# Kernel optimization log

Measured on AMD Instinct MI355X. Metric: run time of the kernel, lower is better.

Reference implementation:

```python
import jax, jax.numpy as jnp
import numpy as np

D_IN, D_HIDDEN, DT_RANK, D_MEM, STEP = 256, 64, 16, 128, 16
B_, L_ = 2, 2048
S = 0.02  # weight init scale

def generate_a(d_in, d_hidden):
    i = jnp.arange(d_in, dtype=jnp.float32)[:, None]
    j = jnp.arange(d_hidden, dtype=jnp.float32)[None, :]
    off = jnp.sqrt(2.0 * i + 1.0) * jnp.sqrt(2.0 * j + 1.0)
    return jnp.where(i == j, i + 1.0, jnp.where(i > j, off, 0.0))

def setup_inputs():
    key = jax.random.key(0)
    ks = jax.random.split(key, 10)
    d_out = 3 * D_HIDDEN + 2 * D_IN + 2 * DT_RANK
    return {
        "x": jax.random.normal(ks[0], (B_, L_, D_IN), jnp.float32),
        "W_xproj": jax.random.normal(ks[1], (D_IN, d_out), jnp.float32) * S,
        "W_dt": jax.random.normal(ks[2], (DT_RANK, D_IN), jnp.float32) * S,
        "b_dt": jnp.full((D_IN,), -11.0, jnp.float32),
        "W_dtl": jax.random.normal(ks[3], (DT_RANK, D_IN), jnp.float32) * S,
        "b_dtl": jnp.full((D_IN,), -11.0, jnp.float32),
        "A": generate_a(D_IN, D_HIDDEN),
        "Dp": jnp.ones((D_IN,), jnp.float32),
        "W_Q": jax.random.normal(ks[4], (D_IN, D_MEM), jnp.float32) * S,
        "b_Q": jnp.zeros((D_MEM,), jnp.float32),
        "W_K": jax.random.normal(ks[5], (D_IN, D_MEM), jnp.float32) * S,
        "b_K": jnp.zeros((D_MEM,), jnp.float32),
        "W_V": jax.random.normal(ks[6], (D_IN, D_MEM), jnp.float32) * S,
        "b_V": jnp.zeros((D_MEM,), jnp.float32),
        "W_O": jax.random.normal(ks[7], (D_MEM, D_IN), jnp.float32) * S,
        "b_O": jnp.zeros((D_IN,), jnp.float32),
    }

def _selective_scan(u, delta, A, Bm, Cm, Dp):
    # u, delta: (b,l,d); A: (d,n); Bm, Cm: (b,l,n)
    dA = jnp.exp(jnp.einsum('bld,dn->bldn', delta, A))          # (b,l,d,n)
    dBu = delta[..., None] * Bm[:, :, None, :] * u[..., None]   # (b,l,d,n)
    def comb(e1, e2):
        a1, b1 = e1
        a2, b2 = e2
        return a2 * a1, a2 * b1 + b2
    _, xs = jax.lax.associative_scan(comb, (dA, dBu), axis=1)   # states (b,l,d,n)
    y = jnp.einsum('bldn,bln->bld', xs, Cm)
    if Dp is not None:
        y = y + u * Dp
    return y

def reference(x, W_xproj, W_dt, b_dt, W_dtl, b_dtl, A, Dp, W_Q, b_Q, W_K, b_K, W_V, b_V, W_O, b_O):
    proj = x @ W_xproj  # (b,l,3n+2d+2r)
    splits = np.cumsum([D_HIDDEN, D_HIDDEN, D_HIDDEN, D_IN, D_IN, DT_RANK]).tolist()
    Bm, Bl, Cm, E, Fg, dt, dtl = jnp.split(proj, splits, axis=-1)
    delta = jax.nn.softplus(dt @ W_dt + b_dt)       # delta_softplus=True folded in
    delta_l = jax.nn.softplus(dtl @ W_dtl + b_dtl)
    y = _selective_scan(x, delta, A, Bm, Cm, Dp)
    y_local = _selective_scan(x, delta_l, A, Bl, jnp.ones_like(Bl), None)  # C=ones, D=None
    memory = y_local[:, ::STEP, :]                  # strided checkpoints (b,m,d)
    Q = x @ W_Q + b_Q
    K = memory @ W_K + b_K
    V = memory @ W_V + b_V
    # note: original scales by sqrt(d_hidden), not sqrt(d_memory)
    w = jax.nn.softmax(jnp.einsum('blm,bkm->blk', Q, K) / jnp.sqrt(jnp.float32(D_HIDDEN)), axis=-1)
    att = jnp.einsum('blk,bkm->blm', w, V) @ W_O + b_O
    return y + att * E + x * Fg
```

## Files before the change

kernel.cpp:

```cpp
#include <hip/hip_runtime.h>
#include <math.h>

#define D_INN 256
#define D_HID 64
#define DTR 16
#define D_MEMM 128
#define BB 2
#define LL 2048
#define NROWS (BB*LL)
#define NPROJ 736
#define NTOT 864
#define SEG 16
#define SEGLEN (LL/SEG)
#define NCHUNK (LL/8)

typedef __attribute__((ext_vector_type(8))) short short8v;
typedef __attribute__((ext_vector_type(4))) float float4v;

static __device__ __forceinline__ unsigned short f2bf(float f) {
    unsigned int u = __float_as_uint(f);
    u += 0x7fff + ((u >> 16) & 1);
    return (unsigned short)(u >> 16);
}

static __device__ __forceinline__ float rdlane(float v, int l) {
    return __uint_as_float(__builtin_amdgcn_readlane(__float_as_uint(v), l));
}

#define PK(g, b, chunk, n, li) (((((size_t)(g)*BB + (b)) * NCHUNK + (chunk)) * 64 + (n)) * 8 + (li))

__global__ __launch_bounds__(256) void k_gemm(const float* __restrict__ x,
        const float* __restrict__ Wx, const float* __restrict__ Wq,
        const float* __restrict__ bq, float* __restrict__ proj,
        float* __restrict__ packed) {
    __shared__ unsigned short As[64][40];
    __shared__ unsigned short Bs[64][40];
    const int t = threadIdx.x;
    const int lane = t & 63, w = t >> 6;
    const int wr = w >> 1, wc = w & 1;
    const int row0 = blockIdx.y * 64, col0 = blockIdx.x * 64;

    float4v acc[2][2];
    #pragma unroll
    for (int i = 0; i < 2; i++)
        #pragma unroll
        for (int j = 0; j < 2; j++) acc[i][j] = (float4v)0.f;

    const int ar = t >> 2, akq = (t & 3) * 8;
    const int bk = t >> 3, bcq = (t & 7) * 8;

    for (int k0 = 0; k0 < D_INN; k0 += 32) {
        float4 a0 = *(const float4*)&x[(size_t)(row0 + ar) * D_INN + k0 + akq];
        float4 a1 = *(const float4*)&x[(size_t)(row0 + ar) * D_INN + k0 + akq + 4];
        float4 b0 = {}, b1 = {};
        int col = col0 + bcq;
        if (col + 8 <= NPROJ) {
            b0 = *(const float4*)&Wx[(size_t)(k0 + bk) * NPROJ + col];
            b1 = *(const float4*)&Wx[(size_t)(k0 + bk) * NPROJ + col + 4];
        } else if (col < NTOT) {
            b0 = *(const float4*)&Wq[(size_t)(k0 + bk) * D_MEMM + (col - NPROJ)];
            b1 = *(const float4*)&Wq[(size_t)(k0 + bk) * D_MEMM + (col - NPROJ) + 4];
        }
        __syncthreads();
        {
            unsigned short av[8] = { f2bf(a0.x), f2bf(a0.y), f2bf(a0.z), f2bf(a0.w),
                                     f2bf(a1.x), f2bf(a1.y), f2bf(a1.z), f2bf(a1.w) };
            *(short8v*)&As[ar][akq] = *(short8v*)av;
            Bs[bcq + 0][bk] = f2bf(b0.x); Bs[bcq + 1][bk] = f2bf(b0.y);
            Bs[bcq + 2][bk] = f2bf(b0.z); Bs[bcq + 3][bk] = f2bf(b0.w);
            Bs[bcq + 4][bk] = f2bf(b1.x); Bs[bcq + 5][bk] = f2bf(b1.y);
            Bs[bcq + 6][bk] = f2bf(b1.z); Bs[bcq + 7][bk] = f2bf(b1.w);
        }
        __syncthreads();
        short8v af[2], bf[2];
        const int fr = lane & 15, fk = (lane >> 4) * 8;
        af[0] = *(short8v*)&As[wr * 32 + fr][fk];
        af[1] = *(short8v*)&As[wr * 32 + 16 + fr][fk];
        bf[0] = *(short8v*)&Bs[wc * 32 + fr][fk];
        bf[1] = *(short8v*)&Bs[wc * 32 + 16 + fr][fk];
        #pragma unroll
        for (int i = 0; i < 2; i++)
            #pragma unroll
            for (int j = 0; j < 2; j++)
                acc[i][j] = __builtin_amdgcn_mfma_f32_16x16x32_bf16(af[i], bf[j], acc[i][j], 0, 0, 0);
    }
    #pragma unroll
    for (int i = 0; i < 2; i++)
        #pragma unroll
        for (int j = 0; j < 2; j++) {
            int cc = col0 + wc * 32 + j * 16 + (lane & 15);
            int rr0 = row0 + wr * 32 + i * 16 + (lane >> 4) * 4;
            if (cc < 192) {
                int g = cc >> 6, n = cc & 63;
                int bb = rr0 >> 11, l = rr0 & (LL - 1);
                float4 pk = make_float4(acc[i][j][0], acc[i][j][1], acc[i][j][2], acc[i][j][3]);
                *(float4*)&packed[PK(g, bb, l >> 3, n, l & 7)] = pk;
            } else {
                #pragma unroll
                for (int e = 0; e < 4; e++) {
                    float v = acc[i][j][e];
                    if (cc >= NPROJ) v += bq[cc - NPROJ];
                    proj[(size_t)(rr0 + e) * NTOT + cc] = v;
                }
            }
        }
}

__global__ __launch_bounds__(256) void k_xt(const float* __restrict__ x,
        float* __restrict__ xT) {
    __shared__ float tile[64][65];
    const int t = threadIdx.x;
    const int lt = blockIdx.x * 64, dt = blockIdx.y * 64, b = blockIdx.z;
    const int c = t & 63, rg = (t >> 6) * 16;
    #pragma unroll
    for (int j = 0; j < 16; ++j)
        tile[rg + j][c] = x[((size_t)b * LL + lt + rg + j) * D_INN + dt + c];
    __syncthreads();
    #pragma unroll
    for (int j = 0; j < 16; ++j)
        xT[((size_t)b * D_INN + dt + rg + j) * LL + lt + c] = tile[c][rg + j];
}

__global__ __launch_bounds__(256) void k_delta(const float* __restrict__ proj,
        const float* __restrict__ Wdt, const float* __restrict__ bdt,
        const float* __restrict__ Wdtl, const float* __restrict__ bdtl,
        float* __restrict__ deltaT, float* __restrict__ deltalT) {
    __shared__ float sdt[16][17], sdtl[16][17];
    const int t = threadIdx.x;
    const int r0 = blockIdx.x * 16;
    const int b = r0 >> 11, l0 = r0 & (LL - 1);
    {
        int r = t >> 4, c = t & 15;
        sdt[r][c]  = proj[(size_t)(r0 + r) * NTOT + 704 + c];
        sdtl[r][c] = proj[(size_t)(r0 + r) * NTOT + 720 + c];
    }
    __syncthreads();
    float w1[DTR], w2[DTR];
    #pragma unroll
    for (int r = 0; r < DTR; r++) {
        w1[r] = Wdt[r * D_INN + t];
        w2[r] = Wdtl[r * D_INN + t];
    }
    const float b1 = bdt[t], b2 = bdtl[t];
    float o1[16], o2[16];
    #pragma unroll
    for (int row = 0; row < 16; ++row) {
        float a1 = b1, a2 = b2;
        #pragma unroll
        for (int r = 0; r < DTR; r++) {
            a1 += sdt[row][r] * w1[r];
            a2 += sdtl[row][r] * w2[r];
        }
        o1[row] = (a1 > 20.f) ? a1 : log1pf(expf(a1));
        o2[row] = (a2 > 20.f) ? a2 : log1pf(expf(a2));
    }
    float* p1 = &deltaT[((size_t)b * D_INN + t) * LL + l0];
    float* p2 = &deltalT[((size_t)b * D_INN + t) * LL + l0];
    #pragma unroll
    for (int j = 0; j < 16; j += 4) {
        *(float4*)&p1[j] = make_float4(o1[j], o1[j+1], o1[j+2], o1[j+3]);
        *(float4*)&p2[j] = make_float4(o2[j], o2[j+1], o2[j+2], o2[j+3]);
    }
}

template<int SCAN>
__global__ __launch_bounds__(256) void k_scan1t(const float* __restrict__ xT,
        const float* __restrict__ packed, const float* __restrict__ A,
        const float* __restrict__ dTall,
        float* __restrict__ Qbuf, float* __restrict__ SDbuf,
        float* __restrict__ cumd, float* __restrict__ mem) {
    const int t = threadIdx.x;
    const int w = t >> 6, n = t & 63;
    const int b = blockIdx.y, seg = blockIdx.z;
    const int d = blockIdx.x * 4 + w;
    const float* dT = dTall + ((size_t)b * D_INN + d) * LL + seg * SEGLEN;
    const float* uT = xT + ((size_t)b * D_INN + d) * LL + seg * SEGLEN;
    const float Aln = A[d * D_HID + n] * 1.44269504f;
    const int lr = n & 7;
    const float* Bp = packed + PK(SCAN, b, seg * 16, 0, 0);

    float s = 0.f, sd = 0.f;
    for (int c = 0; c < 16; ++c) {
        float dvl = dT[c * 8 + lr];
        float pl  = dvl * uT[c * 8 + lr];
        float4 B0 = *(const float4*)&Bp[((size_t)c * 64 + n) * 8];
        float4 B1 = *(const float4*)&Bp[((size_t)c * 64 + n) * 8 + 4];
        float Bv[8] = {B0.x, B0.y, B0.z, B0.w, B1.x, B1.y, B1.z, B1.w};
        {
            float dv = rdlane(dvl, 0), p = rdlane(pl, 0);
            s = fmaf(exp2f(dv * Aln), s, p * Bv[0]);
            sd += dv;
        }
        if (SCAN == 1 && (c & 1) == 0) {
            float v = s;
            #pragma unroll
            for (int off = 32; off >= 1; off >>= 1) v += __shfl_xor(v, off);
            if (n == 0) {
                int k = seg * 8 + (c >> 1);
                mem[((size_t)b * 128 + k) * D_INN + d] = v;
                cumd[(((size_t)b * SEG + seg) * 8 + (c >> 1)) * D_INN + d] = sd;
            }
        }
        #pragma unroll
        for (int li = 1; li < 8; ++li) {
            float dv = rdlane(dvl, li), p = rdlane(pl, li);
            s = fmaf(exp2f(dv * Aln), s, p * Bv[li]);
            sd += dv;
        }
    }
    Qbuf[((((size_t)SCAN * 2 + b) * SEG + seg) * D_INN + d) * 64 + n] = s;
    if (n == 0) SDbuf[(((size_t)SCAN * 2 + b) * SEG + seg) * D_INN + d] = sd;
}

__global__ __launch_bounds__(256) void k_scan2(const float* __restrict__ xT,
        const float* __restrict__ packed, const float* __restrict__ A,
        const float* __restrict__ Dp, const float* __restrict__ deltaT,
        const float* __restrict__ Qbuf, const float* __restrict__ SDbuf,
        float* __restrict__ y) {
    __shared__ float rbuf[4][8][65];
    const int t = threadIdx.x;
    const int w = t >> 6, n = t & 63;
    const int b = blockIdx.y, seg = blockIdx.z;
    const int d = blockIdx.x * 4 + w;
    const size_t rowbase = (size_t)b * LL + (size_t)seg * SEGLEN;
    const float* dT = deltaT + ((size_t)b * D_INN + d) * LL + seg * SEGLEN;
    const float* uT = xT + ((size_t)b * D_INN + d) * LL + seg * SEGLEN;
    const float Aln = A[d * D_HID + n] * 1.44269504f;
    const float Dpv = Dp[d];
    const int lr = n & 7;
    const int rli = n >> 3, g = n & 7;
    const float* Bp = packed + PK(0, b, seg * 16, 0, 0);
    const float* Cp = packed + PK(2, b, seg * 16, 0, 0);

    float s = 0.f;
    for (int k = 0; k < seg; ++k) {
        float sdk = SDbuf[(((size_t)b * SEG + k) * D_INN + d)];
        float Qk = Qbuf[(((size_t)b * SEG + k) * D_INN + d) * 64 + n];
        s = fmaf(exp2f(sdk * Aln), s, Qk);
    }

    for (int c = 0; c < 16; ++c) {
        const size_t l0 = rowbase + c * 8;
        float dvl = dT[c * 8 + lr];
        float uvl = uT[c * 8 + lr];
        float pl = dvl * uvl;
        float4 B0 = *(const float4*)&Bp[((size_t)c * 64 + n) * 8];
        float4 B1 = *(const float4*)&Bp[((size_t)c * 64 + n) * 8 + 4];
        float4 C0 = *(const float4*)&Cp[((size_t)c * 64 + n) * 8];
        float4 C1 = *(const float4*)&Cp[((size_t)c * 64 + n) * 8 + 4];
        float Bv[8] = {B0.x, B0.y, B0.z, B0.w, B1.x, B1.y, B1.z, B1.w};
        float Cv[8] = {C0.x, C0.y, C0.z, C0.w, C1.x, C1.y, C1.z, C1.w};
        #pragma unroll
        for (int li = 0; li < 8; ++li) {
            float dv = rdlane(dvl, li);
            float p  = rdlane(pl, li);
            s = fmaf(exp2f(dv * Aln), s, p * Bv[li]);
            rbuf[w][li][n] = s * Cv[li];
        }
        float acc = 0.f;
        #pragma unroll
        for (int j = 0; j < 8; ++j) acc += rbuf[w][rli][g * 8 + j];
        acc += __shfl_xor(acc, 1);
        acc += __shfl_xor(acc, 2);
        acc += __shfl_xor(acc, 4);
        float uv = __shfl(uvl, rli);
        if (g == 0) {
            y[(l0 + rli) * D_INN + d] = acc + uv * Dpv;
        }
    }
}

__global__ __launch_bounds__(256) void k_sin(const float* __restrict__ A,
        const float* __restrict__ Qbuf, const float* __restrict__ SDbuf,
        float* __restrict__ Sin) {
    const int t = threadIdx.x, w = t >> 6, n = t & 63;
    const int b = blockIdx.y;
    const int d = blockIdx.x * 4 + w;
    const float Aln = A[d * D_HID + n] * 1.44269504f;
    float s = 0.f;
    #pragma unroll
    for (int seg = 0; seg < SEG; ++seg) {
        if (seg > 0) Sin[(((size_t)b * SEG + seg) * D_INN + d) * 64 + n] = s;
        float sdk = SDbuf[((size_t)(2 + b) * SEG + seg) * D_INN + d];
        float Qk = Qbuf[(((size_t)(2 + b) * SEG + seg) * D_INN + d) * 64 + n];
        s = fmaf(exp2f(sdk * Aln), s, Qk);
    }
}

__global__ __launch_bounds__(256) void k_fix(const float* __restrict__ A,
        const float* __restrict__ Sin, const float* __restrict__ cumd,
        float* __restrict__ mem) {
    const int t = threadIdx.x, w = t >> 6, n = t & 63;
    const int k = 8 + blockIdx.y;
    const int b = blockIdx.z;
    const int d = blockIdx.x * 4 + w;
    const int seg = k >> 3;
    const float Aln = A[d * D_HID + n] * 1.44269504f;
    float cum = cumd[((size_t)b * 128 + k) * D_INN + d];
    float sv = Sin[(((size_t)b * SEG + seg) * D_INN + d) * 64 + n];
    float v = exp2f(cum * Aln) * sv;
    #pragma unroll
    for (int off = 32; off >= 1; off >>= 1) v += __shfl_xor(v, off);
    if (n == 0) mem[((size_t)b * 128 + k) * D_INN + d] += v;
}

__global__ __launch_bounds__(128) void k_kvwo(const float* __restrict__ mem,
        const float* __restrict__ Wk, const float* __restrict__ bk,
        const float* __restrict__ Wv, const float* __restrict__ bv,
        const float* __restrict__ Wo,
        float* __restrict__ KT, float* __restrict__ VWo) {
    __shared__ float mrow[256];
    __shared__ float vrow[128];
    const int k = blockIdx.x, b = blockIdx.y;
    const int t = threadIdx.x;
    const float* mr = mem + ((size_t)b * 128 + k) * D_INN;
    mrow[t] = mr[t];
    mrow[t + 128] = mr[t + 128];
    __syncthreads();
    float aK = bk[t], aV = bv[t];
    for (int dd = 0; dd < D_INN; dd++) {
        float m = mrow[dd];
        aK += m * Wk[dd * D_MEMM + t];
        aV += m * Wv[dd * D_MEMM + t];
    }
    KT[((size_t)b * 128 + t) * 128 + k] = aK;
    vrow[t] = aV;
    __syncthreads();
    float a0 = 0.f, a1 = 0.f;
    for (int m = 0; m < 128; ++m) {
        float vm = vrow[m];
        a0 += vm * Wo[(size_t)m * D_INN + t];
        a1 += vm * Wo[(size_t)m * D_INN + t + 128];
    }
    VWo[((size_t)b * 128 + k) * D_INN + t] = a0;
    VWo[((size_t)b * 128 + k) * D_INN + t + 128] = a1;
}

__global__ __launch_bounds__(256) void k_attn(const float* __restrict__ x,
        const float* __restrict__ proj, const float* __restrict__ y,
        const float* __restrict__ KT, const float* __restrict__ VWo,
        const float* __restrict__ bo, float* __restrict__ out) {
    __shared__ float qs[8][132];
    __shared__ float ws[8][132];
    __shared__ float denom[8];
    const int t = threadIdx.x;
    const int b = blockIdx.y;
    const int r0 = blockIdx.x * 8;
    const size_t rowbase = (size_t)b * LL + r0;
    {
        int r = t >> 5, c4 = (t & 31) * 4;
        *(float4*)&qs[r][c4] = *(const float4*)&proj[(rowbase + r) * NTOT + NPROJ + c4];
    }
    __syncthreads();
    {
        const int kk = t & 127, rg = (t >> 7) * 4;
        const float* KTb = KT + (size_t)b * 128 * 128 + kk;
        float acc[4] = {};
        #pragma unroll 8
        for (int m = 0; m < 128; m += 4) {
            float k0 = KTb[(size_t)m * 128];
            float k1 = KTb[(size_t)(m + 1) * 128];
            float k2 = KTb[(size_t)(m + 2) * 128];
            float k3 = KTb[(size_t)(m + 3) * 128];
            #pragma unroll
            for (int r = 0; r < 4; ++r) {
                float4 qv = *(const float4*)&qs[rg + r][m];
                acc[r] += qv.x * k0 + qv.y * k1 + qv.z * k2 + qv.w * k3;
            }
        }
        #pragma unroll
        for (int r = 0; r < 4; ++r) ws[rg + r][kk] = acc[r] * 0.125f;
    }
    __syncthreads();
    {
        const int r = t >> 5, j = t & 31;
        float4 v0 = *(float4*)&ws[r][j * 4];
        float mx = fmaxf(fmaxf(v0.x, v0.y), fmaxf(v0.z, v0.w));
        #pragma unroll
        for (int o = 1; o < 32; o <<= 1) mx = fmaxf(mx, __shfl_xor(mx, o));
        v0.x = expf(v0.x - mx); v0.y = expf(v0.y - mx);
        v0.z = expf(v0.z - mx); v0.w = expf(v0.w - mx);
        float sum = v0.x + v0.y + v0.z + v0.w;
        #pragma unroll
        for (int o = 1; o < 32; o <<= 1) sum += __shfl_xor(sum, o);
        *(float4*)&ws[r][j * 4] = v0;
        if (j == 0) denom[r] = sum;
    }
    __syncthreads();
    {
        const int w = t >> 6, lane = t & 63;
        const int c0 = lane * 4;
        const float* vb = VWo + (size_t)b * 128 * D_INN + c0;
        float acc[2][4] = {};
        #pragma unroll 8
        for (int k = 0; k < 128; k += 2) {
            float4 vw0 = *(const float4*)&vb[(size_t)k * D_INN];
            float4 vw1 = *(const float4*)&vb[(size_t)(k + 1) * D_INN];
            #pragma unroll
            for (int r = 0; r < 2; ++r) {
                float wk0 = ws[w * 2 + r][k];
                float wk1 = ws[w * 2 + r][k + 1];
                acc[r][0] += wk0 * vw0.x + wk1 * vw1.x;
                acc[r][1] += wk0 * vw0.y + wk1 * vw1.y;
                acc[r][2] += wk0 * vw0.z + wk1 * vw1.z;
                acc[r][3] += wk0 * vw0.w + wk1 * vw1.w;
            }
        }
        float4 bov = *(const float4*)&bo[c0];
        #pragma unroll
        for (int r = 0; r < 2; ++r) {
            size_t rr = rowbase + w * 2 + r;
            float dn = 1.f / denom[w * 2 + r];
            float4 yv = *(const float4*)&y[rr * D_INN + c0];
            float4 xv = *(const float4*)&x[rr * D_INN + c0];
            float4 Ev = *(const float4*)&proj[rr * NTOT + 192 + c0];
            float4 Fv = *(const float4*)&proj[rr * NTOT + 448 + c0];
            float4 o;
            o.x = yv.x + (acc[r][0] * dn + bov.x) * Ev.x + xv.x * Fv.x;
            o.y = yv.y + (acc[r][1] * dn + bov.y) * Ev.y + xv.y * Fv.y;
            o.z = yv.z + (acc[r][2] * dn + bov.z) * Ev.z + xv.z * Fv.z;
            o.w = yv.w + (acc[r][3] * dn + bov.w) * Ev.w + xv.w * Fv.w;
            *(float4*)&out[rr * D_INN + c0] = o;
        }
    }
}

extern "C" void kernel_launch(void* const* d_in, const int* in_sizes, int n_in,
                              void* d_out, int out_size, void* d_ws, size_t ws_size,
                              hipStream_t stream) {
    const float* x    = (const float*)d_in[0];
    const float* Wx   = (const float*)d_in[1];
    const float* Wdt  = (const float*)d_in[2];
    const float* bdt  = (const float*)d_in[3];
    const float* Wdtl = (const float*)d_in[4];
    const float* bdtl = (const float*)d_in[5];
    const float* A    = (const float*)d_in[6];
    const float* Dp   = (const float*)d_in[7];
    const float* Wq   = (const float*)d_in[8];
    const float* bq   = (const float*)d_in[9];
    const float* Wk   = (const float*)d_in[10];
    const float* bk   = (const float*)d_in[11];
    const float* Wv   = (const float*)d_in[12];
    const float* bv   = (const float*)d_in[13];
    const float* Wo   = (const float*)d_in[14];
    const float* bo   = (const float*)d_in[15];
    float* out = (float*)d_out;
    float* ws = (float*)d_ws;

    float* proj    = ws;
    float* deltaT  = proj + (size_t)NROWS * NTOT;
    float* deltalT = deltaT + (size_t)NROWS * D_INN;
    float* yb      = deltalT + (size_t)NROWS * D_INN;
    float* mem     = yb + (size_t)NROWS * D_INN;
    float* KTb     = mem + (size_t)BB * 128 * D_INN;
    float* Qbuf    = KTb + (size_t)BB * 128 * D_MEMM;
    float* SDbuf   = Qbuf + (size_t)4 * SEG * D_INN * 64;
    float* cumd    = SDbuf + (size_t)4 * SEG * D_INN;
    float* Sin     = cumd + (size_t)BB * SEG * 8 * D_INN;
    float* VWo     = Sin + (size_t)BB * SEG * D_INN * 64;
    float* xT      = VWo + (size_t)BB * 128 * D_INN;
    float* packed  = xT + (size_t)NROWS * D_INN;

    hipLaunchKernelGGL(k_gemm, dim3(14, 64), dim3(256), 0, stream, x, Wx, Wq, bq, proj, packed);
    hipLaunchKernelGGL(k_xt, dim3(32, 4, 2), dim3(256), 0, stream, x, xT);
    hipLaunchKernelGGL(k_delta, dim3(NROWS / 16), dim3(256), 0, stream,
                       proj, Wdt, bdt, Wdtl, bdtl, deltaT, deltalT);
    hipLaunchKernelGGL(k_scan1t<0>, dim3(64, 2, 16), dim3(256), 0, stream,
                       xT, packed, A, deltaT, Qbuf, SDbuf, cumd, mem);
    hipLaunchKernelGGL(k_scan1t<1>, dim3(64, 2, 16), dim3(256), 0, stream,
                       xT, packed, A, deltalT, Qbuf, SDbuf, cumd, mem);
    hipLaunchKernelGGL(k_scan2, dim3(64, 2, 16), dim3(256), 0, stream,
                       xT, packed, A, Dp, deltaT, Qbuf, SDbuf, yb);
    hipLaunchKernelGGL(k_sin, dim3(64, 2), dim3(256), 0, stream,
                       A, Qbuf, SDbuf, Sin);
    hipLaunchKernelGGL(k_fix, dim3(64, 120, 2), dim3(256), 0, stream,
                       A, Sin, cumd, mem);
    hipLaunchKernelGGL(k_kvwo, dim3(128, 2), dim3(128), 0, stream,
                       mem, Wk, bk, Wv, bv, Wo, KTb, VWo);
    hipLaunchKernelGGL(k_attn, dim3(LL / 8, 2), dim3(256), 0, stream,
                       x, proj, yb, KTb, VWo, bo, out);
}
```

Before: 201.8 us.

## Fuse scan passes and prep kernels to cut launches from ten to six

```diff
diff --git a/kernel.cpp b/kernel.cpp
--- a/kernel.cpp
+++ b/kernel.cpp
@@ -106,80 +106,73 @@
         }
 }
 
-__global__ __launch_bounds__(256) void k_xt(const float* __restrict__ x,
-        float* __restrict__ xT) {
-    __shared__ float tile[64][65];
-    const int t = threadIdx.x;
-    const int lt = blockIdx.x * 64, dt = blockIdx.y * 64, b = blockIdx.z;
-    const int c = t & 63, rg = (t >> 6) * 16;
-    #pragma unroll
-    for (int j = 0; j < 16; ++j)
-        tile[rg + j][c] = x[((size_t)b * LL + lt + rg + j) * D_INN + dt + c];
-    __syncthreads();
-    #pragma unroll
-    for (int j = 0; j < 16; ++j)
-        xT[((size_t)b * D_INN + dt + rg + j) * LL + lt + c] = tile[c][rg + j];
-}
-
-__global__ __launch_bounds__(256) void k_delta(const float* __restrict__ proj,
+__global__ __launch_bounds__(256) void k_prep(const float* __restrict__ x,
+        const float* __restrict__ proj,
         const float* __restrict__ Wdt, const float* __restrict__ bdt,
         const float* __restrict__ Wdtl, const float* __restrict__ bdtl,
-        float* __restrict__ deltaT, float* __restrict__ deltalT) {
-    __shared__ float sdt[16][17], sdtl[16][17];
+        float* __restrict__ deltaT, float* __restrict__ deltalT,
+        float* __restrict__ xT) {
+    __shared__ float sh[64 * 66];
     const int t = threadIdx.x;
-    const int r0 = blockIdx.x * 16;
-    const int b = r0 >> 11, l0 = r0 & (LL - 1);
-    {
-        int r = t >> 4, c = t & 15;
-        sdt[r][c]  = proj[(size_t)(r0 + r) * NTOT + 704 + c];
-        sdtl[r][c] = proj[(size_t)(r0 + r) * NTOT + 720 + c];
-    }
-    __syncthreads();
-    float w1[DTR], w2[DTR];
+    if (blockIdx.y == 0) {
+        float (*sdt)[17]  = (float(*)[17])sh;
+        float (*sdtl)[17] = (float(*)[17])(sh + 16 * 17);
+        const int r0 = blockIdx.x * 16;
+        const int b = r0 >> 11, l0 = r0 & (LL - 1);
+        {
+            int r = t >> 4, c = t & 15;
+            sdt[r][c]  = proj[(size_t)(r0 + r) * NTOT + 704 + c];
+            sdtl[r][c] = proj[(size_t)(r0 + r) * NTOT + 720 + c];
+        }
+        __syncthreads();
+        float w1[DTR], w2[DTR];
+        #pragma unroll
+        for (int r = 0; r < DTR; r++) {
+            w1[r] = Wdt[r * D_INN + t];
+            w2[r] = Wdtl[r * D_INN + t];
+        }
+        const float b1 = bdt[t], b2 = bdtl[t];
+        float o1[16], o2[16];
+        #pragma unroll
+        for (int row = 0; row < 16; ++row) {
+            float a1 = b1, a2 = b2;
+            #pragma unroll
+            for (int r = 0; r < DTR; r++) {
+                a1 += sdt[row][r] * w1[r];
+                a2 += sdtl[row][r] * w2[r];
+            }
+            o1[row] = (a1 > 20.f) ? a1 : log1pf(expf(a1));
+            o2[row] = (a2 > 20.f) ? a2 : log1pf(expf(a2));
+        }
+        float* p1 = &deltaT[((size_t)b * D_INN + t) * LL + l0];
+        float* p2 = &deltalT[((size_t)b * D_INN + t) * LL + l0];
+        #pragma unroll
+        for (int j = 0; j < 16; j += 4) {
+            *(float4*)&p1[j] = make_float4(o1[j], o1[j+1], o1[j+2], o1[j+3]);
+            *(float4*)&p2[j] = make_float4(o2[j], o2[j+1], o2[j+2], o2[j+3]);
+        }
+    } else {
+        float (*tile)[65] = (float(*)[65])sh;
+        const int bx = blockIdx.x;
+        const int lt = (bx & 31) * 64, dt = ((bx >> 5) & 3) * 64, b = bx >> 7;
+        const int c = t & 63, rg = (t >> 6) * 16;
+        #pragma unroll
+        for (int j = 0; j < 16; ++j)
+            tile[rg + j][c] = x[((size_t)b * LL + lt + rg + j) * D_INN + dt + c];
+        __syncthreads();
+        #pragma unroll
+        for (int j = 0; j < 16; ++j)
+            xT[((size_t)b * D_INN + dt + rg + j) * LL + lt + c] = tile[c][rg + j];
+    }
+}
+
+template<bool CK>
+static __device__ __forceinline__ void seg_pass1(
+        const float* __restrict__ dT, const float* __restrict__ uT,
+        const float* __restrict__ Bp, float Aln, int lr, int n,
+        float& sOut, float& sdOut, float* cum, float* part) {
+    float s = 0.f, sd = 0.f;
     #pragma unroll
-    for (int r = 0; r < DTR; r++) {
-        w1[r] = Wdt[r * D_INN + t];
-        w2[r] = Wdtl[r * D_INN + t];
-    }
-    const float b1 = bdt[t], b2 = bdtl[t];
-    float o1[16], o2[16];
-    #pragma unroll
-    for (int row = 0; row < 16; ++row) {
-        float a1 = b1, a2 = b2;
-        #pragma unroll
-        for (int r = 0; r < DTR; r++) {
-            a1 += sdt[row][r] * w1[r];
-            a2 += sdtl[row][r] * w2[r];
-        }
-        o1[row] = (a1 > 20.f) ? a1 : log1pf(expf(a1));
-        o2[row] = (a2 > 20.f) ? a2 : log1pf(expf(a2));
-    }
-    float* p1 = &deltaT[((size_t)b * D_INN + t) * LL + l0];
-    float* p2 = &deltalT[((size_t)b * D_INN + t) * LL + l0];
-    #pragma unroll
-    for (int j = 0; j < 16; j += 4) {
-        *(float4*)&p1[j] = make_float4(o1[j], o1[j+1], o1[j+2], o1[j+3]);
-        *(float4*)&p2[j] = make_float4(o2[j], o2[j+1], o2[j+2], o2[j+3]);
-    }
-}
-
-template<int SCAN>
-__global__ __launch_bounds__(256) void k_scan1t(const float* __restrict__ xT,
-        const float* __restrict__ packed, const float* __restrict__ A,
-        const float* __restrict__ dTall,
-        float* __restrict__ Qbuf, float* __restrict__ SDbuf,
-        float* __restrict__ cumd, float* __restrict__ mem) {
-    const int t = threadIdx.x;
-    const int w = t >> 6, n = t & 63;
-    const int b = blockIdx.y, seg = blockIdx.z;
-    const int d = blockIdx.x * 4 + w;
-    const float* dT = dTall + ((size_t)b * D_INN + d) * LL + seg * SEGLEN;
-    const float* uT = xT + ((size_t)b * D_INN + d) * LL + seg * SEGLEN;
-    const float Aln = A[d * D_HID + n] * 1.44269504f;
-    const int lr = n & 7;
-    const float* Bp = packed + PK(SCAN, b, seg * 16, 0, 0);
-
-    float s = 0.f, sd = 0.f;
     for (int c = 0; c < 16; ++c) {
         float dvl = dT[c * 8 + lr];
         float pl  = dvl * uT[c * 8 + lr];
@@ -191,15 +184,12 @@
             s = fmaf(exp2f(dv * Aln), s, p * Bv[0]);
             sd += dv;
         }
-        if (SCAN == 1 && (c & 1) == 0) {
+        if (CK && (c & 1) == 0) {
             float v = s;
             #pragma unroll
             for (int off = 32; off >= 1; off >>= 1) v += __shfl_xor(v, off);
-            if (n == 0) {
-                int k = seg * 8 + (c >> 1);
-                mem[((size_t)b * 128 + k) * D_INN + d] = v;
-                cumd[(((size_t)b * SEG + seg) * 8 + (c >> 1)) * D_INN + d] = sd;
-            }
+            part[c >> 1] = v;
+            cum[c >> 1] = sd;
         }
         #pragma unroll
         for (int li = 1; li < 8; ++li) {
@@ -208,40 +198,87 @@
             sd += dv;
         }
     }
-    Qbuf[((((size_t)SCAN * 2 + b) * SEG + seg) * D_INN + d) * 64 + n] = s;
-    if (n == 0) SDbuf[(((size_t)SCAN * 2 + b) * SEG + seg) * D_INN + d] = sd;
-}
-
-__global__ __launch_bounds__(256) void k_scan2(const float* __restrict__ xT,
+    sOut = s; sdOut = sd;
+}
+
+__global__ __launch_bounds__(256) void k_scanA(const float* __restrict__ xT,
+        const float* __restrict__ packed, const float* __restrict__ A,
+        const float* __restrict__ deltaT, const float* __restrict__ deltalT,
+        float* __restrict__ Qbuf, float* __restrict__ SDbuf,
+        float* __restrict__ cumd, float* __restrict__ mem) {
+    const int t = threadIdx.x, w = t >> 6, n = t & 63;
+    const int b = blockIdx.y, seg = blockIdx.z;
+    const int d = blockIdx.x * 4 + w;
+    const int lr = n & 7;
+    const float Aln = A[d * D_HID + n] * 1.44269504f;
+    const float* uT  = xT + ((size_t)b * D_INN + d) * LL + seg * SEGLEN;
+    const float* dT0 = deltaT + ((size_t)b * D_INN + d) * LL + seg * SEGLEN;
+    const float* dT1 = deltalT + ((size_t)b * D_INN + d) * LL + seg * SEGLEN;
+
+    float cum[8], part[8];
+    float q0, sd0, q1, sd1;
+    seg_pass1<false>(dT0, uT, packed + PK(0, b, seg * 16, 0, 0), Aln, lr, n,
+                     q0, sd0, nullptr, nullptr);
+    seg_pass1<true>(dT1, uT, packed + PK(1, b, seg * 16, 0, 0), Aln, lr, n,
+                    q1, sd1, cum, part);
+
+    Qbuf[(((size_t)b * SEG + seg) * D_INN + d) * 64 + n] = q0;
+    Qbuf[(((size_t)(2 + b) * SEG + seg) * D_INN + d) * 64 + n] = q1;
+    if (n == 0) {
+        SDbuf[((size_t)b * SEG + seg) * D_INN + d] = sd0;
+        SDbuf[((size_t)(2 + b) * SEG + seg) * D_INN + d] = sd1;
+        #pragma unroll
+        for (int ck = 0; ck < 8; ++ck) {
+            mem[((size_t)b * 128 + seg * 8 + ck) * D_INN + d] = part[ck];
+            cumd[(((size_t)b * SEG + seg) * 8 + ck) * D_INN + d] = cum[ck];
+        }
+    }
+}
+
+__global__ __launch_bounds__(256) void k_scanBC(const float* __restrict__ xT,
         const float* __restrict__ packed, const float* __restrict__ A,
         const float* __restrict__ Dp, const float* __restrict__ deltaT,
         const float* __restrict__ Qbuf, const float* __restrict__ SDbuf,
-        float* __restrict__ y) {
+        const float* __restrict__ cumd,
+        float* __restrict__ y, float* __restrict__ mem) {
     __shared__ float rbuf[4][8][65];
-    const int t = threadIdx.x;
-    const int w = t >> 6, n = t & 63;
+    const int t = threadIdx.x, w = t >> 6, n = t & 63;
     const int b = blockIdx.y, seg = blockIdx.z;
     const int d = blockIdx.x * 4 + w;
-    const size_t rowbase = (size_t)b * LL + (size_t)seg * SEGLEN;
-    const float* dT = deltaT + ((size_t)b * D_INN + d) * LL + seg * SEGLEN;
-    const float* uT = xT + ((size_t)b * D_INN + d) * LL + seg * SEGLEN;
+    const int lr = n & 7, rli = n >> 3, g = n & 7;
     const float Aln = A[d * D_HID + n] * 1.44269504f;
     const float Dpv = Dp[d];
-    const int lr = n & 7;
-    const int rli = n >> 3, g = n & 7;
+    const size_t rowbase = (size_t)b * LL + (size_t)seg * SEGLEN;
+    const float* uT  = xT + ((size_t)b * D_INN + d) * LL + seg * SEGLEN;
+    const float* dT0 = deltaT + ((size_t)b * D_INN + d) * LL + seg * SEGLEN;
     const float* Bp = packed + PK(0, b, seg * 16, 0, 0);
     const float* Cp = packed + PK(2, b, seg * 16, 0, 0);
 
-    float s = 0.f;
+    float sin0 = 0.f, sin1 = 0.f;
     for (int k = 0; k < seg; ++k) {
-        float sdk = SDbuf[(((size_t)b * SEG + k) * D_INN + d)];
-        float Qk = Qbuf[(((size_t)b * SEG + k) * D_INN + d) * 64 + n];
-        s = fmaf(exp2f(sdk * Aln), s, Qk);
-    }
-
+        float sdk0 = SDbuf[((size_t)b * SEG + k) * D_INN + d];
+        float qk0  = Qbuf[(((size_t)b * SEG + k) * D_INN + d) * 64 + n];
+        sin0 = fmaf(exp2f(sdk0 * Aln), sin0, qk0);
+        float sdk1 = SDbuf[((size_t)(2 + b) * SEG + k) * D_INN + d];
+        float qk1  = Qbuf[(((size_t)(2 + b) * SEG + k) * D_INN + d) * 64 + n];
+        sin1 = fmaf(exp2f(sdk1 * Aln), sin1, qk1);
+    }
+
+    if (seg > 0) {
+        #pragma unroll
+        for (int ck = 0; ck < 8; ++ck) {
+            float cum = cumd[(((size_t)b * SEG + seg) * 8 + ck) * D_INN + d];
+            float v = exp2f(cum * Aln) * sin1;
+            #pragma unroll
+            for (int off = 32; off >= 1; off >>= 1) v += __shfl_xor(v, off);
+            if (n == 0) mem[((size_t)b * 128 + seg * 8 + ck) * D_INN + d] += v;
+        }
+    }
+
+    float s = sin0;
     for (int c = 0; c < 16; ++c) {
         const size_t l0 = rowbase + c * 8;
-        float dvl = dT[c * 8 + lr];
+        float dvl = dT0[c * 8 + lr];
         float uvl = uT[c * 8 + lr];
         float pl = dvl * uvl;
         float4 B0 = *(const float4*)&Bp[((size_t)c * 64 + n) * 8];
@@ -268,40 +305,6 @@
             y[(l0 + rli) * D_INN + d] = acc + uv * Dpv;
         }
     }
-}
-
-__global__ __launch_bounds__(256) void k_sin(const float* __restrict__ A,
-        const float* __restrict__ Qbuf, const float* __restrict__ SDbuf,
-        float* __restrict__ Sin) {
-    const int t = threadIdx.x, w = t >> 6, n = t & 63;
-    const int b = blockIdx.y;
-    const int d = blockIdx.x * 4 + w;
-    const float Aln = A[d * D_HID + n] * 1.44269504f;
-    float s = 0.f;
-    #pragma unroll
-    for (int seg = 0; seg < SEG; ++seg) {
-        if (seg > 0) Sin[(((size_t)b * SEG + seg) * D_INN + d) * 64 + n] = s;
-        float sdk = SDbuf[((size_t)(2 + b) * SEG + seg) * D_INN + d];
-        float Qk = Qbuf[(((size_t)(2 + b) * SEG + seg) * D_INN + d) * 64 + n];
-        s = fmaf(exp2f(sdk * Aln), s, Qk);
-    }
-}
-
-__global__ __launch_bounds__(256) void k_fix(const float* __restrict__ A,
-        const float* __restrict__ Sin, const float* __restrict__ cumd,
-        float* __restrict__ mem) {
-    const int t = threadIdx.x, w = t >> 6, n = t & 63;
-    const int k = 8 + blockIdx.y;
-    const int b = blockIdx.z;
-    const int d = blockIdx.x * 4 + w;
-    const int seg = k >> 3;
-    const float Aln = A[d * D_HID + n] * 1.44269504f;
-    float cum = cumd[((size_t)b * 128 + k) * D_INN + d];
-    float sv = Sin[(((size_t)b * SEG + seg) * D_INN + d) * 64 + n];
-    float v = exp2f(cum * Aln) * sv;
-    #pragma unroll
-    for (int off = 32; off >= 1; off >>= 1) v += __shfl_xor(v, off);
-    if (n == 0) mem[((size_t)b * 128 + k) * D_INN + d] += v;
 }
 
 __global__ __launch_bounds__(128) void k_kvwo(const float* __restrict__ mem,
@@ -456,25 +459,17 @@
     float* Qbuf    = KTb + (size_t)BB * 128 * D_MEMM;
     float* SDbuf   = Qbuf + (size_t)4 * SEG * D_INN * 64;
     float* cumd    = SDbuf + (size_t)4 * SEG * D_INN;
-    float* Sin     = cumd + (size_t)BB * SEG * 8 * D_INN;
-    float* VWo     = Sin + (size_t)BB * SEG * D_INN * 64;
+    float* VWo     = cumd + (size_t)BB * SEG * 8 * D_INN;
     float* xT      = VWo + (size_t)BB * 128 * D_INN;
     float* packed  = xT + (size_t)NROWS * D_INN;
 
     hipLaunchKernelGGL(k_gemm, dim3(14, 64), dim3(256), 0, stream, x, Wx, Wq, bq, proj, packed);
-    hipLaunchKernelGGL(k_xt, dim3(32, 4, 2), dim3(256), 0, stream, x, xT);
-    hipLaunchKernelGGL(k_delta, dim3(NROWS / 16), dim3(256), 0, stream,
-                       proj, Wdt, bdt, Wdtl, bdtl, deltaT, deltalT);
-    hipLaunchKernelGGL(k_scan1t<0>, dim3(64, 2, 16), dim3(256), 0, stream,
-                       xT, packed, A, deltaT, Qbuf, SDbuf, cumd, mem);
-    hipLaunchKernelGGL(k_scan1t<1>, dim3(64, 2, 16), dim3(256), 0, stream,
-                       xT, packed, A, deltalT, Qbuf, SDbuf, cumd, mem);
-    hipLaunchKernelGGL(k_scan2, dim3(64, 2, 16), dim3(256), 0, stream,
-                       xT, packed, A, Dp, deltaT, Qbuf, SDbuf, yb);
-    hipLaunchKernelGGL(k_sin, dim3(64, 2), dim3(256), 0, stream,
-                       A, Qbuf, SDbuf, Sin);
-    hipLaunchKernelGGL(k_fix, dim3(64, 120, 2), dim3(256), 0, stream,
-                       A, Sin, cumd, mem);
+    hipLaunchKernelGGL(k_prep, dim3(256, 2), dim3(256), 0, stream,
+                       x, proj, Wdt, bdt, Wdtl, bdtl, deltaT, deltalT, xT);
+    hipLaunchKernelGGL(k_scanA, dim3(64, 2, 16), dim3(256), 0, stream,
+                       xT, packed, A, deltaT, deltalT, Qbuf, SDbuf, cumd, mem);
+    hipLaunchKernelGGL(k_scanBC, dim3(64, 2, 16), dim3(256), 0, stream,
+                       xT, packed, A, Dp, deltaT, Qbuf, SDbuf, cumd, yb, mem);
     hipLaunchKernelGGL(k_kvwo, dim3(128, 2), dim3(128), 0, stream,
                        mem, Wk, bk, Wv, bv, Wo, KTb, VWo);
     hipLaunchKernelGGL(k_attn, dim3(LL / 8, 2), dim3(256), 0, stream,
```

New measurement: 195.2 us. 3.2% less time.
